# Kernel tuning notes

Measured on AMD Instinct MI355X. Metric: run time of the kernel, lower is better.

Reference implementation:

```python
import jax, jax.numpy as jnp
import numpy as np
from math import factorial

L_MAX = 3
K = 256
N = 2048


def _cg_coeff(l1, m1, l2, m2, l3, m3):
    # Clebsch-Gordan coefficient <l1 m1 l2 m2 | l3 m3> via the Racah formula.
    if m3 != m1 + m2:
        return 0.0
    pref = ((2 * l3 + 1) * factorial(l3 + l1 - l2) * factorial(l3 - l1 + l2)
            * factorial(l1 + l2 - l3) / factorial(l1 + l2 + l3 + 1)) ** 0.5
    pref *= (factorial(l3 + m3) * factorial(l3 - m3) * factorial(l1 - m1)
             * factorial(l1 + m1) * factorial(l2 - m2) * factorial(l2 + m2)) ** 0.5
    s = 0.0
    for k in range(0, l1 + l2 - l3 + 1):
        d = [k, l1 + l2 - l3 - k, l1 - m1 - k, l2 + m2 - k,
             l3 - l2 + m1 + k, l3 - l1 - m2 + k]
        if min(d) < 0:
            continue
        den = 1.0
        for x in d:
            den *= factorial(x)
        s += (-1.0) ** k / den
    return pref * s


def _cg_tensor(l1, l2, l3):
    out = np.zeros((2 * l1 + 1, 2 * l2 + 1, 2 * l3 + 1), dtype=np.float32)
    for m1 in range(-l1, l1 + 1):
        for m2 in range(-l2, l2 + 1):
            m3 = m1 + m2
            if -l3 <= m3 <= l3:
                out[m1 + l1, m2 + l2, m3 + l3] = _cg_coeff(l1, m1, l2, m2, l3, m3)
    return jnp.asarray(out)


# All (l1, l2) -> l coupling paths allowed by the triangle inequality, l <= L_MAX.
PATHS = {l: [(l1, l2) for l1 in range(L_MAX + 1) for l2 in range(L_MAX + 1)
             if abs(l1 - l2) <= l <= l1 + l2] for l in range(L_MAX + 1)}
CG = {(l1, l2, l): _cg_tensor(l1, l2, l)
      for l in range(L_MAX + 1) for (l1, l2) in PATHS[l]}


def _forward(f1, f2, U, W):
    outs = []
    for l in range(L_MAX + 1):
        # CG tensor product: elementwise over channels k, coupled over (m1, m2) -> m.
        parts = [jnp.einsum('abm,nak,nbk->nmk', CG[(l1, l2, l)], f1[l1], f2[l2])
                 for (l1, l2) in PATHS[l]]
        tp = jnp.concatenate(parts, axis=-1)          # [N, 2l+1, n_paths(l)*K]
        mixed = jnp.einsum('nmc,ck->nmk', tp, U[l])   # U_dict per-l mixing -> [N, 2l+1, K]
        mixed = jnp.einsum('nmk,kj->nmj', mixed, W[l])  # learned per-l linear
        outs.append(f1[l] + mixed)                    # residual
    return tuple(outs)


def setup_inputs() -> dict:
    key = jax.random.key(0)
    ks = jax.random.split(key, 16)
    inp = {}
    for l in range(L_MAX + 1):
        inp[f'f1_l{l}'] = jax.random.normal(ks[l], (N, 2 * l + 1, K), jnp.float32)
        inp[f'f2_l{l}'] = jax.random.normal(ks[4 + l], (N, 2 * l + 1, K), jnp.float32)
        cin = len(PATHS[l]) * K
        inp[f'U_{l}'] = jax.random.normal(ks[8 + l], (cin, K), jnp.float32) / float(np.sqrt(cin))
        inp[f'W_{l}'] = jax.random.normal(ks[12 + l], (K, K), jnp.float32) / float(np.sqrt(K))
    return inp


def reference(f1_l0, f1_l1, f1_l2, f1_l3,
              f2_l0, f2_l1, f2_l2, f2_l3,
              U_0, U_1, U_2, U_3,
              W_0, W_1, W_2, W_3):
    f1 = [f1_l0, f1_l1, f1_l2, f1_l3]
    f2 = [f2_l0, f2_l1, f2_l2, f2_l3]
    U = [U_0, U_1, U_2, U_3]
    W = [W_0, W_1, W_2, W_3]
    return _forward(f1, f2, U, W)
```

## Files before the change

### kernel.cpp

```cpp
#include <hip/hip_runtime.h>
#include <math.h>

typedef __attribute__((ext_vector_type(4))) float f32x4;
typedef __attribute__((ext_vector_type(2))) float f32x2;
typedef __attribute__((ext_vector_type(8))) __bf16 bf16x8;
typedef __attribute__((ext_vector_type(4))) __bf16 bf16x4;
typedef __attribute__((ext_vector_type(2))) __bf16 bf16x2;

__device__ __constant__ int GP_L[34]  = {0,0,0,0, 1,1,1,1,1,1,1,1,1, 2,2,2,2,2,2,2,2,2,2,2, 3,3,3,3,3,3,3,3,3,3};
__device__ __constant__ int GP_L1[34] = {0,1,2,3, 0,1,1,1,2,2,2,3,3, 0,1,1,1,2,2,2,2,3,3,3, 0,1,1,2,2,2,3,3,3,3};
__device__ __constant__ int GP_L2[34] = {0,1,2,3, 1,0,1,2,1,2,3,2,3, 2,1,2,3,0,1,2,3,1,2,3, 3,2,3,1,2,3,0,1,2,3};

__device__ double dfact(int n) { double r = 1.0; for (int i = 2; i <= n; ++i) r *= (double)i; return r; }

__device__ double cg_coeff(int l1, int m1, int l2, int m2, int l3, int m3) {
  if (m3 != m1 + m2) return 0.0;
  double pref = sqrt((2.0 * l3 + 1.0) * dfact(l3 + l1 - l2) * dfact(l3 - l1 + l2)
                     * dfact(l1 + l2 - l3) / dfact(l1 + l2 + l3 + 1));
  pref *= sqrt(dfact(l3 + m3) * dfact(l3 - m3) * dfact(l1 - m1) * dfact(l1 + m1)
               * dfact(l2 - m2) * dfact(l2 + m2));
  double s = 0.0;
  for (int k = 0; k <= l1 + l2 - l3; ++k) {
    int d0 = k, d1 = l1 + l2 - l3 - k, d2 = l1 - m1 - k, d3 = l2 + m2 - k;
    int d4 = l3 - l2 + m1 + k, d5 = l3 - l1 - m2 + k;
    if (d0 < 0 || d1 < 0 || d2 < 0 || d3 < 0 || d4 < 0 || d5 < 0) continue;
    double den = dfact(d0) * dfact(d1) * dfact(d2) * dfact(d3) * dfact(d4) * dfact(d5);
    s += ((k & 1) ? -1.0 : 1.0) / den;
  }
  return pref * s;
}

__global__ __launch_bounds__(256) void prep(
    const float* __restrict__ u0, const float* __restrict__ u1,
    const float* __restrict__ u2, const float* __restrict__ u3,
    const float* __restrict__ w0, const float* __restrict__ w1,
    const float* __restrict__ w2, const float* __restrict__ w3,
    __bf16* __restrict__ Ubf, __bf16* __restrict__ Wt, float* __restrict__ cg) {
  const int bid = blockIdx.x, tid = threadIdx.x;
  if (bid < 2176) {
    long i = (long)bid * 256 + tid;
    const long b1 = 65536, b2 = 212992, b3 = 393216;
    const float* src; long s;
    if (i < b1)      { src = u0; s = i; }
    else if (i < b2) { src = u1; s = i - b1; }
    else if (i < b3) { src = u2; s = i - b2; }
    else             { src = u3; s = i - b3; }
    float4 v = ((const float4*)src)[s];
    bf16x4 o;
    o[0] = (__bf16)v.x; o[1] = (__bf16)v.y; o[2] = (__bf16)v.z; o[3] = (__bf16)v.w;
    ((bf16x4*)Ubf)[i] = o;
  } else if (bid < 3200) {
    int b = bid - 2176;
    int l = b >> 8, j = b & 255;
    const float* W = (l == 0) ? w0 : (l == 1) ? w1 : (l == 2) ? w2 : w3;
    Wt[((long)l << 16) + (j << 8) + tid] = (__bf16)W[(tid << 8) + j];
  } else {
    int idx = (bid - 3200) * 256 + tid;
    if (idx < 34 * 49) {
      int gp = idx / 49, r = idx % 49;
      int m1i = r / 7, m2i = r % 7;
      int l3 = GP_L[gp], l1 = GP_L1[gp], l2 = GP_L2[gp];
      float v = 0.f;
      if (m1i <= 2 * l1 && m2i <= 2 * l2) {
        int m1 = m1i - l1, m2 = m2i - l2, m3 = m1 + m2;
        if (m3 >= -l3 && m3 <= l3) v = (float)cg_coeff(l1, m1, l2, m2, l3, m3);
      }
      cg[idx] = v;
    }
  }
}

struct GemmDesc {
  const __bf16* A[4];
  const __bf16* B[4];
  __bf16*       C[4];
  int start[4];
  int lmap[4];
  int Kd[4];
  int Nc[4];
};

__device__ __forceinline__ void gload_lds16(const void* g, void* l) {
  __builtin_amdgcn_global_load_lds((const __attribute__((address_space(1))) void*)g,
                                   (__attribute__((address_space(3))) void*)l, 16, 0, 0);
}

__device__ void uw_body(const GemmDesc& d, int bid, char* sm) {
  const int tid = threadIdx.x;
  int seg = 0;
  if (bid >= d.start[1]) seg = 1;
  if (bid >= d.start[2]) seg = 2;
  if (bid >= d.start[3]) seg = 3;
  const int l = d.lmap[seg];
  const int rel = bid - d.start[seg];
  const int Kd = d.Kd[l], Nc = d.Nc[l];
  const int nTN = Nc >> 7;
  const int tM = rel / nTN, tN = rel % nTN;

  const int lane = tid & 63, wave = tid >> 6;
  const int wm = (wave >> 1) << 6, wn = (wave & 1) << 6;
  const int lr = lane & 15, lk = (lane >> 4) << 3;

  f32x4 acc[4][4] = {};

  const int r32 = tid >> 3;
  const int sl = ((tid & 7) ^ (r32 & 7)) << 3;
  const __bf16* Ag = d.A[l] + (long)(tM * 128 + r32) * Kd + sl;
  const __bf16* Bg = d.B[l] + (long)(tN * 128 + r32) * Kd + sl;
  char* AsB = sm;
  char* BsB = sm + 16384;

  for (int kt = 0; kt < Kd; kt += 64) {
#pragma unroll
    for (int i = 0; i < 4; ++i) {
      gload_lds16(Ag + (long)i * 32 * Kd + kt, AsB + i * 4096 + tid * 16);
      gload_lds16(Bg + (long)i * 32 * Kd + kt, BsB + i * 4096 + tid * 16);
    }
    __syncthreads();

#pragma unroll
    for (int kk = 0; kk < 64; kk += 32) {
      bf16x8 af[4], bq[4];
#pragma unroll
      for (int mi = 0; mi < 4; ++mi)
        af[mi] = *(const bf16x8*)(AsB + ((wm + mi * 16 + lr) << 7)
                                      + ((((kk + lk) << 1)) ^ ((lr & 7) << 4)));
#pragma unroll
      for (int ni = 0; ni < 4; ++ni)
        bq[ni] = *(const bf16x8*)(BsB + ((wn + ni * 16 + lr) << 7)
                                      + ((((kk + lk) << 1)) ^ ((lr & 7) << 4)));
#pragma unroll
      for (int mi = 0; mi < 4; ++mi)
#pragma unroll
        for (int ni = 0; ni < 4; ++ni)
          acc[mi][ni] = __builtin_amdgcn_mfma_f32_16x16x32_bf16(af[mi], bq[ni], acc[mi][ni], 0, 0, 0);
    }
    __syncthreads();
  }

  const long col0 = (long)tN * 128 + wn + lr;
  const long row0 = (long)tM * 128 + wm + ((lane >> 4) << 2);
#pragma unroll
  for (int mi = 0; mi < 4; ++mi)
#pragma unroll
    for (int j = 0; j < 4; ++j) {
      long r = row0 + mi * 16 + j;
      long base = r * (long)Nc + col0;
#pragma unroll
      for (int ni = 0; ni < 4; ++ni)
        d.C[l][base + ni * 16] = (__bf16)acc[mi][ni][j];
    }
}

#define TPW2(LV, DST, CIN, GOFF, P, L1V, L2V)                                    \
  { f32x2 tp[2 * (LV) + 1];                                                      \
    _Pragma("unroll") for (int m = 0; m <= 2 * (LV); ++m) { tp[m][0] = 0.f; tp[m][1] = 0.f; } \
    const float* cgt = cg + ((GOFF) + (P)) * 49;                                 \
    _Pragma("unroll") for (int a = 0; a <= 2 * (L1V); ++a)                       \
      _Pragma("unroll") for (int b = 0; b <= 2 * (L2V); ++b) {                   \
        const int m = a + b - ((L1V) + (L2V) - (LV));                            \
        if (m >= 0 && m <= 2 * (LV)) {                                           \
          float c = cgt[a * 7 + b];                                              \
          tp[m][0] = fmaf(c, v1[CUM[L1V] + a][0] * v2[CUM[L2V] + b][0], tp[m][0]); \
          tp[m][1] = fmaf(c, v1[CUM[L1V] + a][1] * v2[CUM[L2V] + b][1], tp[m][1]); \
        } }                                                                      \
    __bf16* o = (DST) + (n * (2 * (LV) + 1)) * (CIN) + (P) * 256 + k2;           \
    _Pragma("unroll") for (int m = 0; m <= 2 * (LV); ++m) {                      \
      bf16x2 ov; ov[0] = (__bf16)tp[m][0]; ov[1] = (__bf16)tp[m][1];             \
      *(bf16x2*)(o + (long)m * (CIN)) = ov; } }

template <int LMASK>
__device__ void tp_body(
    const float* __restrict__ f10, const float* __restrict__ f11,
    const float* __restrict__ f12, const float* __restrict__ f13,
    const float* __restrict__ f20, const float* __restrict__ f21,
    const float* __restrict__ f22, const float* __restrict__ f23,
    const float* __restrict__ cg,
    __bf16* __restrict__ A0, __bf16* __restrict__ A1,
    __bf16* __restrict__ A2, __bf16* __restrict__ A3, int bid) {
  const int tid = threadIdx.x;
  const long n = (long)bid * 2 + (tid >> 7);
  const int k2 = (tid & 127) << 1;
  constexpr int CUM[4] = {0, 1, 4, 9};
  const float* f1s[4] = {f10, f11, f12, f13};
  const float* f2s[4] = {f20, f21, f22, f23};

  f32x2 v1[16], v2[16];
#pragma unroll
  for (int l1 = 0; l1 < 4; ++l1) {
    const float* p1 = f1s[l1] + (n * (2 * l1 + 1)) * 256 + k2;
    const float* p2 = f2s[l1] + (n * (2 * l1 + 1)) * 256 + k2;
#pragma unroll
    for (int a = 0; a <= 2 * l1; ++a) {
      v1[CUM[l1] + a] = *(const f32x2*)(p1 + (long)a * 256);
      v2[CUM[l1] + a] = *(const f32x2*)(p2 + (long)a * 256);
    }
  }

  if constexpr (LMASK & 1) {
    TPW2(0, A0, 1024, 0, 0, 0, 0)  TPW2(0, A0, 1024, 0, 1, 1, 1)
    TPW2(0, A0, 1024, 0, 2, 2, 2)  TPW2(0, A0, 1024, 0, 3, 3, 3)
  }
  if constexpr (LMASK & 2) {
    TPW2(1, A1, 2304, 4, 0, 0, 1)  TPW2(1, A1, 2304, 4, 1, 1, 0)
    TPW2(1, A1, 2304, 4, 2, 1, 1)  TPW2(1, A1, 2304, 4, 3, 1, 2)
    TPW2(1, A1, 2304, 4, 4, 2, 1)  TPW2(1, A1, 2304, 4, 5, 2, 2)
    TPW2(1, A1, 2304, 4, 6, 2, 3)  TPW2(1, A1, 2304, 4, 7, 3, 2)
    TPW2(1, A1, 2304, 4, 8, 3, 3)
  }
  if constexpr (LMASK & 4) {
    TPW2(2, A2, 2816, 13, 0, 0, 2)  TPW2(2, A2, 2816, 13, 1, 1, 1)
    TPW2(2, A2, 2816, 13, 2, 1, 2)  TPW2(2, A2, 2816, 13, 3, 1, 3)
    TPW2(2, A2, 2816, 13, 4, 2, 0)  TPW2(2, A2, 2816, 13, 5, 2, 1)
    TPW2(2, A2, 2816, 13, 6, 2, 2)  TPW2(2, A2, 2816, 13, 7, 2, 3)
    TPW2(2, A2, 2816, 13, 8, 3, 1)  TPW2(2, A2, 2816, 13, 9, 3, 2)
    TPW2(2, A2, 2816, 13, 10, 3, 3)
  }
  if constexpr (LMASK & 8) {
    TPW2(3, A3, 2560, 24, 0, 0, 3)  TPW2(3, A3, 2560, 24, 1, 1, 2)
    TPW2(3, A3, 2560, 24, 2, 1, 3)  TPW2(3, A3, 2560, 24, 3, 2, 1)
    TPW2(3, A3, 2560, 24, 4, 2, 2)  TPW2(3, A3, 2560, 24, 5, 2, 3)
    TPW2(3, A3, 2560, 24, 6, 3, 0)  TPW2(3, A3, 2560, 24, 7, 3, 1)
    TPW2(3, A3, 2560, 24, 8, 3, 2)  TPW2(3, A3, 2560, 24, 9, 3, 3)
  }
}

template <int LMASK>
__global__ __launch_bounds__(256) void tp_uw(
    const float* __restrict__ f10, const float* __restrict__ f11,
    const float* __restrict__ f12, const float* __restrict__ f13,
    const float* __restrict__ f20, const float* __restrict__ f21,
    const float* __restrict__ f22, const float* __restrict__ f23,
    const float* __restrict__ cg,
    __bf16* __restrict__ A0, __bf16* __restrict__ A1,
    __bf16* __restrict__ A2, __bf16* __restrict__ A3,
    GemmDesc gd, int nUW) {
  __shared__ __align__(16) char sm[32768];
  const int bid = (int)blockIdx.x;
  if (bid < nUW) {
    uw_body(gd, bid, sm);
  } else if constexpr (LMASK != 0) {
    tp_body<LMASK>(f10, f11, f12, f13, f20, f21, f22, f23, cg,
                   A0, A1, A2, A3, bid - nUW);
  }
}

struct MainDesc {
  const __bf16* A[4];
  const __bf16* B[4];
  float*        C[4];
  const float*  R[4];
  int start[4];
  int lmap[4];
  int cin4[4];
};

__global__ __launch_bounds__(512) void gemm_main(MainDesc d) {
  __shared__ __align__(16) char sm[147456];
  const int tid = threadIdx.x;
  int bid;
  {
    const int cpx = gridDim.x >> 3;
    bid = ((int)blockIdx.x & 7) * cpx + ((int)blockIdx.x >> 3);
  }
  int seg = 0;
  if (bid >= d.start[1]) seg = 1;
  if (bid >= d.start[2]) seg = 2;
  if (bid >= d.start[3]) seg = 3;
  const int l = d.lmap[seg];
  const int tM = bid - d.start[seg];
  const int cin = d.cin4[l];
  const int NT = cin >> 6;

  const __bf16* __restrict__ Aseg = d.A[l] + (long)tM * 128 * cin;
  const __bf16* __restrict__ Bseg = d.B[l];

  const int srow = tid >> 3;
  const int sx = ((tid & 7) ^ (srow & 7)) << 3;

  const int lane = tid & 63, wave = tid >> 6;
  const int wm = (wave >> 2) << 6;
  const int wn = (wave & 3) << 6;
  const int lr = lane & 15, lkb = (lane >> 4) << 3;

  f32x4 acc[4][4];
#pragma unroll
  for (int i = 0; i < 4; ++i)
#pragma unroll
    for (int j = 0; j < 4; ++j) { acc[i][j][0]=0.f; acc[i][j][1]=0.f; acc[i][j][2]=0.f; acc[i][j][3]=0.f; }

#define STAGE(s, t)                                                              \
  { char* base_ = sm + (s) * 49152;                                              \
    const long kt_ = (long)(t) << 6;                                             \
    _Pragma("unroll")                                                            \
    for (int i = 0; i < 2; ++i)                                                  \
      gload_lds16(Aseg + (long)(i * 64 + srow) * cin + kt_ + sx,                 \
                  base_ + i * 8192 + tid * 16);                                  \
    _Pragma("unroll")                                                            \
    for (int i = 0; i < 4; ++i)                                                  \
      gload_lds16(Bseg + (long)(i * 64 + srow) * cin + kt_ + sx,                 \
                  base_ + 16384 + i * 8192 + tid * 16); }

  STAGE(0, 0)
  STAGE(1, 1)

  for (int t = 0; t < NT; ++t) {
    if (t + 2 < NT) {
      STAGE((t + 2) % 3, t + 2)
      asm volatile("s_waitcnt vmcnt(12)" ::: "memory");
    } else if (t + 2 == NT) {
      asm volatile("s_waitcnt vmcnt(6)" ::: "memory");
    } else {
      asm volatile("s_waitcnt vmcnt(0)" ::: "memory");
    }
    __builtin_amdgcn_s_barrier();
    __builtin_amdgcn_sched_barrier(0);

    const char* Ab = sm + (t % 3) * 49152;
    const char* Bb = Ab + 16384;
    __builtin_amdgcn_s_setprio(1);
#pragma unroll
    for (int kk = 0; kk < 64; kk += 32) {
      bf16x8 af[4], bq[4];
#pragma unroll
      for (int mi = 0; mi < 4; ++mi) {
        const int row = wm + mi * 16 + lr;
        af[mi] = *(const bf16x8*)(Ab + row * 128 + ((((kk + lkb) << 1)) ^ ((row & 7) << 4)));
      }
#pragma unroll
      for (int ni = 0; ni < 4; ++ni) {
        const int row = wn + ni * 16 + lr;
        bq[ni] = *(const bf16x8*)(Bb + row * 128 + ((((kk + lkb) << 1)) ^ ((row & 7) << 4)));
      }
#pragma unroll
      for (int mi = 0; mi < 4; ++mi)
#pragma unroll
        for (int ni = 0; ni < 4; ++ni)
          acc[mi][ni] = __builtin_amdgcn_mfma_f32_16x16x32_bf16(af[mi], bq[ni], acc[mi][ni], 0, 0, 0);
    }
    __builtin_amdgcn_s_setprio(0);
    __builtin_amdgcn_sched_barrier(0);
    __builtin_amdgcn_s_barrier();
  }
#undef STAGE

  float* __restrict__ Cout = d.C[l];
  const float* __restrict__ Resid = d.R[l];
  const int rb = (lane >> 4) << 2;
#pragma unroll
  for (int mi = 0; mi < 4; ++mi)
#pragma unroll
    for (int j = 0; j < 4; ++j) {
      const long row = (long)tM * 128 + wm + mi * 16 + rb + j;
      const long base = row * 256 + wn + lr;
#pragma unroll
      for (int ni = 0; ni < 4; ++ni)
        Cout[base + ni * 16] = acc[mi][ni][j] + Resid[base + ni * 16];
    }
}

extern "C" void kernel_launch(void* const* d_in, const int* in_sizes, int n_in,
                              void* d_out, int out_size, void* d_ws, size_t ws_size,
                              hipStream_t stream) {
  const float* F1[4], * F2[4], * Uin[4], * Win[4];
  for (int l = 0; l < 4; ++l) {
    F1[l]  = (const float*)d_in[4 * l + 0];
    F2[l]  = (const float*)d_in[4 * l + 1];
    Uin[l] = (const float*)d_in[4 * l + 2];
    Win[l] = (const float*)d_in[4 * l + 3];
  }
  static const int  cin_[4]  = {1024, 2304, 2816, 2560};
  static const int  cum_[4]  = {0, 1024, 3328, 6144};
  static const long moff_[4] = {0, 524288, 2097152, 4718592};
  static const int  nTM_[4]  = {16, 48, 80, 112};
  static const long asz_[4]  = {4194304L, 28311552L, 57671680L, 73400320L};

  char* ws = (char*)d_ws;
  float*  cg   = (float*)ws;
  __bf16* Ubf  = (__bf16*)(ws + 8192);
  __bf16* Wtbf = (__bf16*)(ws + 8192 + 4456448);
  __bf16* UWt  = (__bf16*)(ws + 5242880);
  const long ABASE = 10485760;
  const bool big = ws_size >= (size_t)(ABASE + asz_[0] + asz_[1] + asz_[2] + asz_[3]);

  __bf16* Ab[4];
  if (big) {
    long off = ABASE;
    for (int l = 0; l < 4; ++l) { Ab[l] = (__bf16*)(ws + off); off += asz_[l]; }
  } else {
    for (int l = 0; l < 4; ++l) Ab[l] = (__bf16*)(ws + ABASE);
  }

  hipLaunchKernelGGL(prep, dim3(3207), dim3(256), 0, stream,
                     Uin[0], Uin[1], Uin[2], Uin[3],
                     Win[0], Win[1], Win[2], Win[3], Ubf, Wtbf, cg);

  GemmDesc gd;
  {
    int starts[4] = {0, 40, 84, 120};
    int lmap[4]   = {3, 2, 1, 0};
    for (int s = 0; s < 4; ++s) { gd.start[s] = starts[s]; gd.lmap[s] = lmap[s]; }
    for (int l = 0; l < 4; ++l) {
      gd.A[l] = Wtbf + (long)l * 65536;
      gd.B[l] = Ubf + (long)cum_[l] * 256;
      gd.C[l] = UWt + (long)cum_[l] * 256;
      gd.Kd[l] = 256;
      gd.Nc[l] = cin_[l];
    }
  }

  if (big) {
    hipLaunchKernelGGL((tp_uw<15>), dim3(1160), dim3(256), 0, stream,
                       F1[0], F1[1], F1[2], F1[3], F2[0], F2[1], F2[2], F2[3],
                       cg, Ab[0], Ab[1], Ab[2], Ab[3], gd, 136);
    MainDesc d;
    int starts[4] = {0, 112, 192, 240};
    int lmap[4]   = {3, 2, 1, 0};
    for (int s = 0; s < 4; ++s) { d.start[s] = starts[s]; d.lmap[s] = lmap[s]; }
    for (int l = 0; l < 4; ++l) {
      d.A[l] = Ab[l];
      d.B[l] = UWt + (long)cum_[l] * 256;
      d.C[l] = (float*)d_out + moff_[l];
      d.R[l] = F1[l];
      d.cin4[l] = cin_[l];
    }
    hipLaunchKernelGGL(gemm_main, dim3(256), dim3(512), 0, stream, d);
  } else {
    hipLaunchKernelGGL((tp_uw<0>), dim3(136), dim3(256), 0, stream,
                       F1[0], F1[1], F1[2], F1[3], F2[0], F2[1], F2[2], F2[3],
                       cg, Ab[0], Ab[1], Ab[2], Ab[3], gd, 136);
    for (int l = 0; l < 4; ++l) {
      switch (l) {
        case 0: hipLaunchKernelGGL((tp_uw<1>), dim3(1024), dim3(256), 0, stream,
                  F1[0],F1[1],F1[2],F1[3], F2[0],F2[1],F2[2],F2[3], cg,
                  Ab[0],Ab[1],Ab[2],Ab[3], gd, 0); break;
        case 1: hipLaunchKernelGGL((tp_uw<2>), dim3(1024), dim3(256), 0, stream,
                  F1[0],F1[1],F1[2],F1[3], F2[0],F2[1],F2[2],F2[3], cg,
                  Ab[0],Ab[1],Ab[2],Ab[3], gd, 0); break;
        case 2: hipLaunchKernelGGL((tp_uw<4>), dim3(1024), dim3(256), 0, stream,
                  F1[0],F1[1],F1[2],F1[3], F2[0],F2[1],F2[2],F2[3], cg,
                  Ab[0],Ab[1],Ab[2],Ab[3], gd, 0); break;
        case 3: hipLaunchKernelGGL((tp_uw<8>), dim3(1024), dim3(256), 0, stream,
                  F1[0],F1[1],F1[2],F1[3], F2[0],F2[1],F2[2],F2[3], cg,
                  Ab[0],Ab[1],Ab[2],Ab[3], gd, 0); break;
      }
      MainDesc d;
      for (int s = 0; s < 4; ++s) {
        d.start[s] = (s == 0) ? 0 : 0x7fffffff;
        d.lmap[s] = l;
      }
      for (int ll = 0; ll < 4; ++ll) {
        d.A[ll] = Ab[l];
        d.B[ll] = UWt + (long)cum_[l] * 256;
        d.C[ll] = (float*)d_out + moff_[l];
        d.R[ll] = F1[l];
        d.cin4[ll] = cin_[l];
      }
      hipLaunchKernelGGL(gemm_main, dim3(nTM_[l]), dim3(512), 0, stream, d);
    }
  }
  (void)in_sizes; (void)n_in; (void)out_size; (void)ws_size;
}
```

Measured before the change: 142.7 us.

## Shrink GEMM K-tile and LDS to double buffer for higher occupancy

Reduces the main GEMM's LDS footprint from a three-stage 64-wide K pipeline to a two-stage 32-wide K double buffer and adds a launch-bounds hint for multiple blocks per CU. It also rewrites the LDS swizzle for the narrower tile. The intent is to let more blocks reside per CU to hide memory latency, at the cost of a shallower prefetch pipeline, twice as many barriers, and possible register-pressure spills.

```diff
diff --git a/kernel.cpp b/kernel.cpp
--- a/kernel.cpp
+++ b/kernel.cpp
@@ -255,8 +255,8 @@
   int cin4[4];
 };
 
-__global__ __launch_bounds__(512) void gemm_main(MainDesc d) {
-  __shared__ __align__(16) char sm[147456];
+__global__ __launch_bounds__(512, 4) void gemm_main(MainDesc d) {
+  __shared__ __align__(16) char sm[49152];
   const int tid = threadIdx.x;
   int bid;
   {
@@ -270,18 +270,23 @@
   const int l = d.lmap[seg];
   const int tM = bid - d.start[seg];
   const int cin = d.cin4[l];
-  const int NT = cin >> 6;
+  const int NT = cin >> 5;
 
   const __bf16* __restrict__ Aseg = d.A[l] + (long)tM * 128 * cin;
   const __bf16* __restrict__ Bseg = d.B[l];
 
-  const int srow = tid >> 3;
-  const int sx = ((tid & 7) ^ (srow & 7)) << 3;
+  const int arow = tid >> 2;
+  const int asx = (((tid & 3) ^ ((tid >> 3) & 3)) << 3);
+  const int brow0 = tid >> 2;
+  const int bsx0 = asx;
+  const int brow1 = (512 + tid) >> 2;
+  const int bsx1 = (((tid & 3) ^ (((512 + tid) >> 3) & 3)) << 3);
 
   const int lane = tid & 63, wave = tid >> 6;
   const int wm = (wave >> 2) << 6;
   const int wn = (wave & 3) << 6;
-  const int lr = lane & 15, lkb = (lane >> 4) << 3;
+  const int lr = lane & 15;
+  const int lslot = lane >> 4;
 
   f32x4 acc[4][4];
 #pragma unroll
@@ -290,57 +295,37 @@
     for (int j = 0; j < 4; ++j) { acc[i][j][0]=0.f; acc[i][j][1]=0.f; acc[i][j][2]=0.f; acc[i][j][3]=0.f; }
 
 #define STAGE(s, t)                                                              \
-  { char* base_ = sm + (s) * 49152;                                              \
-    const long kt_ = (long)(t) << 6;                                             \
-    _Pragma("unroll")                                                            \
-    for (int i = 0; i < 2; ++i)                                                  \
-      gload_lds16(Aseg + (long)(i * 64 + srow) * cin + kt_ + sx,                 \
-                  base_ + i * 8192 + tid * 16);                                  \
-    _Pragma("unroll")                                                            \
-    for (int i = 0; i < 4; ++i)                                                  \
-      gload_lds16(Bseg + (long)(i * 64 + srow) * cin + kt_ + sx,                 \
-                  base_ + 16384 + i * 8192 + tid * 16); }
+  { char* base_ = sm + (s) * 24576;                                              \
+    const long kt_ = (long)(t) << 5;                                             \
+    gload_lds16(Aseg + (long)arow * cin + kt_ + asx, base_ + tid * 16);          \
+    gload_lds16(Bseg + (long)brow0 * cin + kt_ + bsx0, base_ + 8192 + tid * 16); \
+    gload_lds16(Bseg + (long)brow1 * cin + kt_ + bsx1, base_ + 8192 + 8192 + tid * 16); }
 
   STAGE(0, 0)
-  STAGE(1, 1)
+  __syncthreads();
 
   for (int t = 0; t < NT; ++t) {
-    if (t + 2 < NT) {
-      STAGE((t + 2) % 3, t + 2)
-      asm volatile("s_waitcnt vmcnt(12)" ::: "memory");
-    } else if (t + 2 == NT) {
-      asm volatile("s_waitcnt vmcnt(6)" ::: "memory");
-    } else {
-      asm volatile("s_waitcnt vmcnt(0)" ::: "memory");
-    }
-    __builtin_amdgcn_s_barrier();
-    __builtin_amdgcn_sched_barrier(0);
-
-    const char* Ab = sm + (t % 3) * 49152;
-    const char* Bb = Ab + 16384;
-    __builtin_amdgcn_s_setprio(1);
-#pragma unroll
-    for (int kk = 0; kk < 64; kk += 32) {
-      bf16x8 af[4], bq[4];
-#pragma unroll
-      for (int mi = 0; mi < 4; ++mi) {
-        const int row = wm + mi * 16 + lr;
-        af[mi] = *(const bf16x8*)(Ab + row * 128 + ((((kk + lkb) << 1)) ^ ((row & 7) << 4)));
-      }
-#pragma unroll
-      for (int ni = 0; ni < 4; ++ni) {
-        const int row = wn + ni * 16 + lr;
-        bq[ni] = *(const bf16x8*)(Bb + row * 128 + ((((kk + lkb) << 1)) ^ ((row & 7) << 4)));
-      }
-#pragma unroll
-      for (int mi = 0; mi < 4; ++mi)
-#pragma unroll
-        for (int ni = 0; ni < 4; ++ni)
-          acc[mi][ni] = __builtin_amdgcn_mfma_f32_16x16x32_bf16(af[mi], bq[ni], acc[mi][ni], 0, 0, 0);
-    }
-    __builtin_amdgcn_s_setprio(0);
-    __builtin_amdgcn_sched_barrier(0);
-    __builtin_amdgcn_s_barrier();
+    const int cur = t & 1;
+    if (t + 1 < NT) STAGE(cur ^ 1, t + 1)
+    const char* Ab = sm + cur * 24576;
+    const char* Bb = Ab + 8192;
+    bf16x8 af[4], bq[4];
+#pragma unroll
+    for (int mi = 0; mi < 4; ++mi) {
+      const int row = wm + mi * 16 + lr;
+      af[mi] = *(const bf16x8*)(Ab + row * 64 + ((lslot ^ ((row >> 1) & 3)) << 4));
+    }
+#pragma unroll
+    for (int ni = 0; ni < 4; ++ni) {
+      const int row = wn + ni * 16 + lr;
+      bq[ni] = *(const bf16x8*)(Bb + row * 64 + ((lslot ^ ((row >> 1) & 3)) << 4));
+    }
+#pragma unroll
+    for (int mi = 0; mi < 4; ++mi)
+#pragma unroll
+      for (int ni = 0; ni < 4; ++ni)
+        acc[mi][ni] = __builtin_amdgcn_mfma_f32_16x16x32_bf16(af[mi], bq[ni], acc[mi][ni], 0, 0, 0);
+    __syncthreads();
   }
 #undef STAGE
 
```

Result: no change. 141.7 us (-0.7%).

## Retile main GEMM to 256x128 blocks with split-phase prefetch interleaving

Applied to the files above, without the earlier changes.

The main GEMM tile changes from 128x256 (M x N) to 256x128, with each block covering one of two N halves. The 8 waves become a 4x2 grid. The K-loop now loads LDS fragments for each 32-wide half-step, then issues half of the next stage's global-to-LDS loads, then runs the MFMAs, so memory issue is spread across compute phases. Segment order is changed so l=2 blocks come first. The barrier count per iteration rises, and the wait counts are hand-tuned, so miscounted vmcnt values are a correctness risk.

```diff
diff --git a/kernel.cpp b/kernel.cpp
--- a/kernel.cpp
+++ b/kernel.cpp
@@ -268,20 +268,24 @@
   if (bid >= d.start[2]) seg = 2;
   if (bid >= d.start[3]) seg = 3;
   const int l = d.lmap[seg];
-  const int tM = bid - d.start[seg];
+  const int rel = bid - d.start[seg];
+  const int tM = rel >> 1, tN = rel & 1;
   const int cin = d.cin4[l];
   const int NT = cin >> 6;
 
-  const __bf16* __restrict__ Aseg = d.A[l] + (long)tM * 128 * cin;
-  const __bf16* __restrict__ Bseg = d.B[l];
+  const __bf16* __restrict__ Aseg = d.A[l] + (long)tM * 256 * cin;
+  const __bf16* __restrict__ Bseg = d.B[l] + (long)tN * 128 * cin;
 
   const int srow = tid >> 3;
-  const int sx = ((tid & 7) ^ (srow & 7)) << 3;
+  const int sx = (((tid & 7) ^ ((tid >> 3) & 7)) << 3);
 
   const int lane = tid & 63, wave = tid >> 6;
-  const int wm = (wave >> 2) << 6;
-  const int wn = (wave & 3) << 6;
+  const int wm = (wave >> 1) << 6;
+  const int wn = (wave & 1) << 6;
   const int lr = lane & 15, lkb = (lane >> 4) << 3;
+  const int xorb = (lr & 7) << 4;
+  const int aoff = (wm + lr) << 7;
+  const int boff = (wn + lr) << 7;
 
   f32x4 acc[4][4];
 #pragma unroll
@@ -289,70 +293,91 @@
 #pragma unroll
     for (int j = 0; j < 4; ++j) { acc[i][j][0]=0.f; acc[i][j][1]=0.f; acc[i][j][2]=0.f; acc[i][j][3]=0.f; }
 
-#define STAGE(s, t)                                                              \
-  { char* base_ = sm + (s) * 49152;                                              \
-    const long kt_ = (long)(t) << 6;                                             \
-    _Pragma("unroll")                                                            \
-    for (int i = 0; i < 2; ++i)                                                  \
-      gload_lds16(Aseg + (long)(i * 64 + srow) * cin + kt_ + sx,                 \
-                  base_ + i * 8192 + tid * 16);                                  \
-    _Pragma("unroll")                                                            \
-    for (int i = 0; i < 4; ++i)                                                  \
-      gload_lds16(Bseg + (long)(i * 64 + srow) * cin + kt_ + sx,                 \
-                  base_ + 16384 + i * 8192 + tid * 16); }
-
-  STAGE(0, 0)
-  STAGE(1, 1)
+#define SG_A3(s, t)                                                              \
+  { char* b_ = sm + (s) * 49152; const long kt_ = (long)(t) << 6;                \
+    gload_lds16(Aseg + (long)(  0 + srow) * cin + kt_ + sx, b_ +     0 + tid * 16); \
+    gload_lds16(Aseg + (long)( 64 + srow) * cin + kt_ + sx, b_ +  8192 + tid * 16); \
+    gload_lds16(Aseg + (long)(128 + srow) * cin + kt_ + sx, b_ + 16384 + tid * 16); }
+#define SG_REST(s, t)                                                            \
+  { char* b_ = sm + (s) * 49152; const long kt_ = (long)(t) << 6;                \
+    gload_lds16(Aseg + (long)(192 + srow) * cin + kt_ + sx, b_ + 24576 + tid * 16); \
+    gload_lds16(Bseg + (long)(  0 + srow) * cin + kt_ + sx, b_ + 32768 + tid * 16); \
+    gload_lds16(Bseg + (long)( 64 + srow) * cin + kt_ + sx, b_ + 40960 + tid * 16); }
+
+  SG_A3(0, 0) SG_REST(0, 0)
+  SG_A3(1, 1) SG_REST(1, 1)
+  asm volatile("s_waitcnt vmcnt(6)" ::: "memory");
+  __builtin_amdgcn_s_barrier();
+  __builtin_amdgcn_sched_barrier(0);
 
   for (int t = 0; t < NT; ++t) {
-    if (t + 2 < NT) {
-      STAGE((t + 2) % 3, t + 2)
-      asm volatile("s_waitcnt vmcnt(12)" ::: "memory");
-    } else if (t + 2 == NT) {
-      asm volatile("s_waitcnt vmcnt(6)" ::: "memory");
-    } else {
-      asm volatile("s_waitcnt vmcnt(0)" ::: "memory");
-    }
+    const char* Ab = sm + (t % 3) * 49152;
+    const char* Bb = Ab + 32768;
+    const bool pf = (t + 2 < NT);
+    const int ns = (t + 2) % 3;
+    bf16x8 af[4], bq[4];
+
+    {
+      const int kb = ((lkb << 1)) ^ xorb;
+#pragma unroll
+      for (int mi = 0; mi < 4; ++mi) af[mi] = *(const bf16x8*)(Ab + aoff + mi * 2048 + kb);
+#pragma unroll
+      for (int ni = 0; ni < 4; ++ni) bq[ni] = *(const bf16x8*)(Bb + boff + ni * 2048 + kb);
+    }
+    if (pf) SG_A3(ns, t + 2)
+    __builtin_amdgcn_sched_barrier(0);
     __builtin_amdgcn_s_barrier();
-    __builtin_amdgcn_sched_barrier(0);
-
-    const char* Ab = sm + (t % 3) * 49152;
-    const char* Bb = Ab + 16384;
+    asm volatile("s_waitcnt lgkmcnt(0)" ::: "memory");
+    __builtin_amdgcn_sched_barrier(0);
     __builtin_amdgcn_s_setprio(1);
 #pragma unroll
-    for (int kk = 0; kk < 64; kk += 32) {
-      bf16x8 af[4], bq[4];
-#pragma unroll
-      for (int mi = 0; mi < 4; ++mi) {
-        const int row = wm + mi * 16 + lr;
-        af[mi] = *(const bf16x8*)(Ab + row * 128 + ((((kk + lkb) << 1)) ^ ((row & 7) << 4)));
-      }
-#pragma unroll
-      for (int ni = 0; ni < 4; ++ni) {
-        const int row = wn + ni * 16 + lr;
-        bq[ni] = *(const bf16x8*)(Bb + row * 128 + ((((kk + lkb) << 1)) ^ ((row & 7) << 4)));
-      }
-#pragma unroll
-      for (int mi = 0; mi < 4; ++mi)
-#pragma unroll
-        for (int ni = 0; ni < 4; ++ni)
-          acc[mi][ni] = __builtin_amdgcn_mfma_f32_16x16x32_bf16(af[mi], bq[ni], acc[mi][ni], 0, 0, 0);
-    }
+    for (int mi = 0; mi < 4; ++mi)
+#pragma unroll
+      for (int ni = 0; ni < 4; ++ni)
+        acc[mi][ni] = __builtin_amdgcn_mfma_f32_16x16x32_bf16(af[mi], bq[ni], acc[mi][ni], 0, 0, 0);
     __builtin_amdgcn_s_setprio(0);
     __builtin_amdgcn_sched_barrier(0);
     __builtin_amdgcn_s_barrier();
-  }
-#undef STAGE
+    __builtin_amdgcn_sched_barrier(0);
+
+    {
+      const int kb = (((32 + lkb) << 1)) ^ xorb;
+#pragma unroll
+      for (int mi = 0; mi < 4; ++mi) af[mi] = *(const bf16x8*)(Ab + aoff + mi * 2048 + kb);
+#pragma unroll
+      for (int ni = 0; ni < 4; ++ni) bq[ni] = *(const bf16x8*)(Bb + boff + ni * 2048 + kb);
+    }
+    if (pf) SG_REST(ns, t + 2)
+    __builtin_amdgcn_sched_barrier(0);
+    __builtin_amdgcn_s_barrier();
+    asm volatile("s_waitcnt lgkmcnt(0)" ::: "memory");
+    __builtin_amdgcn_sched_barrier(0);
+    __builtin_amdgcn_s_setprio(1);
+#pragma unroll
+    for (int mi = 0; mi < 4; ++mi)
+#pragma unroll
+      for (int ni = 0; ni < 4; ++ni)
+        acc[mi][ni] = __builtin_amdgcn_mfma_f32_16x16x32_bf16(af[mi], bq[ni], acc[mi][ni], 0, 0, 0);
+    __builtin_amdgcn_s_setprio(0);
+    __builtin_amdgcn_sched_barrier(0);
+    if (t < NT - 2)       asm volatile("s_waitcnt vmcnt(6)" ::: "memory");
+    else if (t == NT - 2) asm volatile("s_waitcnt vmcnt(0)" ::: "memory");
+    __builtin_amdgcn_s_barrier();
+    __builtin_amdgcn_sched_barrier(0);
+  }
+#undef SG_A3
+#undef SG_REST
 
   float* __restrict__ Cout = d.C[l];
   const float* __restrict__ Resid = d.R[l];
   const int rb = (lane >> 4) << 2;
+  const int col0 = tN * 128 + wn + lr;
 #pragma unroll
   for (int mi = 0; mi < 4; ++mi)
 #pragma unroll
     for (int j = 0; j < 4; ++j) {
-      const long row = (long)tM * 128 + wm + mi * 16 + rb + j;
-      const long base = row * 256 + wn + lr;
+      const long row = (long)tM * 256 + wm + mi * 16 + rb + j;
+      const long base = row * 256 + col0;
 #pragma unroll
       for (int ni = 0; ni < 4; ++ni)
         Cout[base + ni * 16] = acc[mi][ni][j] + Resid[base + ni * 16];
@@ -372,7 +397,7 @@
   static const int  cin_[4]  = {1024, 2304, 2816, 2560};
   static const int  cum_[4]  = {0, 1024, 3328, 6144};
   static const long moff_[4] = {0, 524288, 2097152, 4718592};
-  static const int  nTM_[4]  = {16, 48, 80, 112};
+  static const int  nBLK_[4] = {16, 48, 80, 112};
   static const long asz_[4]  = {4194304L, 28311552L, 57671680L, 73400320L};
 
   char* ws = (char*)d_ws;
@@ -414,8 +439,8 @@
                        F1[0], F1[1], F1[2], F1[3], F2[0], F2[1], F2[2], F2[3],
                        cg, Ab[0], Ab[1], Ab[2], Ab[3], gd, 136);
     MainDesc d;
-    int starts[4] = {0, 112, 192, 240};
-    int lmap[4]   = {3, 2, 1, 0};
+    int starts[4] = {0, 80, 192, 240};
+    int lmap[4]   = {2, 3, 1, 0};
     for (int s = 0; s < 4; ++s) { d.start[s] = starts[s]; d.lmap[s] = lmap[s]; }
     for (int l = 0; l < 4; ++l) {
       d.A[l] = Ab[l];
@@ -456,7 +481,7 @@
         d.R[ll] = F1[l];
         d.cin4[ll] = cin_[l];
       }
-      hipLaunchKernelGGL(gemm_main, dim3(nTM_[l]), dim3(512), 0, stream, d);
+      hipLaunchKernelGGL(gemm_main, dim3(nBLK_[l]), dim3(512), 0, stream, d);
     }
   }
   (void)in_sizes; (void)n_in; (void)out_size; (void)ws_size;
```

After: 128.0 us, median of 2. -10.3%, faster.

## Replace triple-buffered LDS pipeline with double buffering in main GEMM

Applied to the files above, without the earlier changes.

The main GEMM kernel moves from a 3-stage LDS ring (prefetch two tiles ahead, fine-grained vmcnt waits, setprio) to a 2-stage double buffer that prefetches one tile ahead and syncs with __syncthreads each iteration. LDS use drops from 144KB to 96KB. The prefetch depth shrinks and the explicit waitcnt/priority scheduling goes away, so global-load latency is less hidden. Only one 512-thread block fits per CU either way, so the smaller LDS footprint is unlikely to raise occupancy.

```diff
diff --git a/kernel.cpp b/kernel.cpp
--- a/kernel.cpp
+++ b/kernel.cpp
@@ -256,7 +256,7 @@
 };
 
 __global__ __launch_bounds__(512) void gemm_main(MainDesc d) {
-  __shared__ __align__(16) char sm[147456];
+  __shared__ __align__(16) char sm[98304];
   const int tid = threadIdx.x;
   int bid;
   {
@@ -278,47 +278,36 @@
   const int srow = tid >> 3;
   const int sx = ((tid & 7) ^ (srow & 7)) << 3;
 
+  f32x4 acc[4][4] = {};
+
   const int lane = tid & 63, wave = tid >> 6;
   const int wm = (wave >> 2) << 6;
   const int wn = (wave & 3) << 6;
   const int lr = lane & 15, lkb = (lane >> 4) << 3;
 
-  f32x4 acc[4][4];
+#pragma unroll
+  for (int i = 0; i < 2; ++i)
+    gload_lds16(Aseg + (long)(i * 64 + srow) * cin + sx, sm + i * 8192 + tid * 16);
 #pragma unroll
   for (int i = 0; i < 4; ++i)
-#pragma unroll
-    for (int j = 0; j < 4; ++j) { acc[i][j][0]=0.f; acc[i][j][1]=0.f; acc[i][j][2]=0.f; acc[i][j][3]=0.f; }
-
-#define STAGE(s, t)                                                              \
-  { char* base_ = sm + (s) * 49152;                                              \
-    const long kt_ = (long)(t) << 6;                                             \
-    _Pragma("unroll")                                                            \
-    for (int i = 0; i < 2; ++i)                                                  \
-      gload_lds16(Aseg + (long)(i * 64 + srow) * cin + kt_ + sx,                 \
-                  base_ + i * 8192 + tid * 16);                                  \
-    _Pragma("unroll")                                                            \
-    for (int i = 0; i < 4; ++i)                                                  \
-      gload_lds16(Bseg + (long)(i * 64 + srow) * cin + kt_ + sx,                 \
-                  base_ + 16384 + i * 8192 + tid * 16); }
-
-  STAGE(0, 0)
-  STAGE(1, 1)
+    gload_lds16(Bseg + (long)(i * 64 + srow) * cin + sx, sm + 32768 + i * 8192 + tid * 16);
+  __syncthreads();
 
   for (int t = 0; t < NT; ++t) {
-    if (t + 2 < NT) {
-      STAGE((t + 2) % 3, t + 2)
-      asm volatile("s_waitcnt vmcnt(12)" ::: "memory");
-    } else if (t + 2 == NT) {
-      asm volatile("s_waitcnt vmcnt(6)" ::: "memory");
-    } else {
-      asm volatile("s_waitcnt vmcnt(0)" ::: "memory");
-    }
-    __builtin_amdgcn_s_barrier();
-    __builtin_amdgcn_sched_barrier(0);
-
-    const char* Ab = sm + (t % 3) * 49152;
-    const char* Bb = Ab + 16384;
-    __builtin_amdgcn_s_setprio(1);
+    const int cur = t & 1;
+    if (t + 1 < NT) {
+      const int ktn = (t + 1) << 6;
+      char* An = sm + (cur ^ 1) * 16384;
+      char* Bn = sm + 32768 + (cur ^ 1) * 32768;
+#pragma unroll
+      for (int i = 0; i < 2; ++i)
+        gload_lds16(Aseg + (long)(i * 64 + srow) * cin + ktn + sx, An + i * 8192 + tid * 16);
+#pragma unroll
+      for (int i = 0; i < 4; ++i)
+        gload_lds16(Bseg + (long)(i * 64 + srow) * cin + ktn + sx, Bn + i * 8192 + tid * 16);
+    }
+    const char* Ab = sm + cur * 16384;
+    const char* Bb = sm + 32768 + cur * 32768;
 #pragma unroll
     for (int kk = 0; kk < 64; kk += 32) {
       bf16x8 af[4], bq[4];
@@ -338,21 +327,19 @@
         for (int ni = 0; ni < 4; ++ni)
           acc[mi][ni] = __builtin_amdgcn_mfma_f32_16x16x32_bf16(af[mi], bq[ni], acc[mi][ni], 0, 0, 0);
     }
-    __builtin_amdgcn_s_setprio(0);
-    __builtin_amdgcn_sched_barrier(0);
-    __builtin_amdgcn_s_barrier();
-  }
-#undef STAGE
+    __syncthreads();
+  }
 
   float* __restrict__ Cout = d.C[l];
   const float* __restrict__ Resid = d.R[l];
+  const int col0 = wn + lr;
   const int rb = (lane >> 4) << 2;
 #pragma unroll
   for (int mi = 0; mi < 4; ++mi)
 #pragma unroll
     for (int j = 0; j < 4; ++j) {
       const long row = (long)tM * 128 + wm + mi * 16 + rb + j;
-      const long base = row * 256 + wn + lr;
+      const long base = row * 256 + col0;
 #pragma unroll
       for (int ni = 0; ni < 4; ++ni)
         Cout[base + ni * 16] = acc[mi][ni][j] + Resid[base + ni * 16];
```

Measured after the change: 150.7 us. 5.6% more time.
